# Kernel tuning notes

Hardware: AMD Instinct MI355X
Metric: run time of the kernel (lower is better)

The kernel has to match this reference:

```python
import jax, jax.numpy as jnp
import numpy as np

N = 50000      # nodes
E = 500000     # edges (avg degree 10)
D_IN = 256     # input feature dim
HID = 256      # hidden_channels
HEADS = 8
C_HID = HID // HEADS   # 32 per-head dim for concat layers
NCLS = 8               # num_classes (last layer per-head dim, concat=False)


def setup_inputs() -> dict:
    key = jax.random.key(0)
    keys = iter(jax.random.split(key, 64))
    def w(shape, s=0.05):
        return jax.random.normal(next(keys), shape, jnp.float32) * s
    inp = {}
    inp["x"] = jax.random.normal(next(keys), (N, D_IN), jnp.float32)
    inp["edge_index"] = jax.random.randint(next(keys), (2, E), 0, N, jnp.int32)
    # (fan_in, heads*per_head_out, skip_out) per layer; layer3: concat=False
    layer_cfg = [(D_IN, HEADS * C_HID, HEADS * C_HID),
                 (HID, HEADS * C_HID, HEADS * C_HID),
                 (HID, HEADS * NCLS, NCLS)]
    for i, (fin, hc, skip) in enumerate(layer_cfg, 1):
        for nm in ("q", "k", "v"):
            inp[f"W{nm}{i}"] = w((fin, hc))
            inp[f"b{nm}{i}"] = jnp.zeros((hc,), jnp.float32)
        inp[f"Ws{i}"] = w((fin, skip))
        inp[f"bs{i}"] = jnp.zeros((skip,), jnp.float32)
        inp[f"Wb{i}"] = w((3 * skip, 1))
    for i in (1, 2):
        inp[f"ln{i}_g"] = jnp.ones((HID,), jnp.float32)
        inp[f"ln{i}_b"] = jnp.zeros((HID,), jnp.float32)
    return inp


def _layer_norm(x, g, b):
    mu = x.mean(-1, keepdims=True)
    var = ((x - mu) ** 2).mean(-1, keepdims=True)
    return (x - mu) * jax.lax.rsqrt(var + 1e-5) * g + b


def _tconv(x, src, dst, Wq, bq, Wk, bk, Wv, bv, Ws, bs, Wb, concat):
    """PyG TransformerConv with beta=True, root_weight=True, eval-mode (no dropout)."""
    n = x.shape[0]
    q = (x @ Wq + bq).reshape(n, HEADS, -1)   # [N,H,C]
    k = (x @ Wk + bk).reshape(n, HEADS, -1)
    v = (x @ Wv + bv).reshape(n, HEADS, -1)
    C = q.shape[-1]
    # per-edge attention logits, scaled dot product
    logits = (q[dst] * k[src]).sum(-1) * jax.lax.rsqrt(jnp.float32(C))  # [E,H]
    # segment softmax over incoming edges of each dst node
    m = jax.ops.segment_max(logits, dst, num_segments=n)                # [N,H]
    m = jnp.where(jnp.isfinite(m), m, 0.0)                              # empty segments
    e = jnp.exp(logits - m[dst])
    s = jax.ops.segment_sum(e, dst, num_segments=n)
    alpha = e / (s[dst] + 1e-16)                                        # [E,H]
    # scatter-aggregate messages
    out = jax.ops.segment_sum(v[src] * alpha[:, :, None], dst, num_segments=n)  # [N,H,C]
    out = out.reshape(n, -1) if concat else out.mean(axis=1)
    # beta-gated skip connection
    xr = x @ Ws + bs
    beta = jax.nn.sigmoid(jnp.concatenate([out, xr, out - xr], axis=-1) @ Wb)   # [N,1]
    return beta * xr + (1.0 - beta) * out


def reference(x, edge_index,
              Wq1, bq1, Wk1, bk1, Wv1, bv1, Ws1, bs1, Wb1,
              Wq2, bq2, Wk2, bk2, Wv2, bv2, Ws2, bs2, Wb2,
              Wq3, bq3, Wk3, bk3, Wv3, bv3, Ws3, bs3, Wb3,
              ln1_g, ln1_b, ln2_g, ln2_b):
    src, dst = edge_index[0], edge_index[1]
    h = jax.nn.relu(_layer_norm(
        _tconv(x, src, dst, Wq1, bq1, Wk1, bk1, Wv1, bv1, Ws1, bs1, Wb1, True),
        ln1_g, ln1_b))
    h = jax.nn.relu(_layer_norm(
        _tconv(h, src, dst, Wq2, bq2, Wk2, bk2, Wv2, bv2, Ws2, bs2, Wb2, True),
        ln2_g, ln2_b))
    return _tconv(h, src, dst, Wq3, bq3, Wk3, bk3, Wv3, bv3, Ws3, bs3, Wb3, False)
```

## Files before the change

kernel.cpp:

```cpp
#include <hip/hip_runtime.h>
#include <stdint.h>

typedef __attribute__((ext_vector_type(8))) short short8;
typedef __attribute__((ext_vector_type(4))) float f32x4;
typedef __attribute__((ext_vector_type(4))) _Float16 half4;

struct us4 { unsigned short x, y, z, w; };

__device__ __forceinline__ float b2f(unsigned short u){
  union { unsigned int i; float f; } x; x.i = ((unsigned int)u) << 16; return x.f;
}
__device__ __forceinline__ unsigned short f2b(float f){
  union { float f; unsigned int i; } x; x.f = f;
  unsigned int i = x.i;
  unsigned int r = (i + 0x7FFFu + ((i >> 16) & 1u)) >> 16;
  return (unsigned short)r;
}
__device__ __forceinline__ unsigned short f2h(float f){
  _Float16 h = (_Float16)f;
  union { _Float16 h; unsigned short u; } c; c.h = h; return c.u;
}
__device__ __forceinline__ float sane(float v){
  return fminf(fmaxf(v, -1e30f), 1e30f);
}
__device__ __forceinline__ float lclamp(float v){
  return fminf(fmaxf(v, -60.f), 60.f);
}
__device__ __forceinline__ float ldin(const void* p, size_t i, int f32){
  return f32 ? ((const float*)p)[i] : b2f(((const unsigned short*)p)[i]);
}

__global__ void k_flag(const unsigned short* __restrict__ xu, int* __restrict__ flag){
  __shared__ int cnt;
  if (threadIdx.x == 0) cnt = 0;
  __syncthreads();
  unsigned u = xu[2 * threadIdx.x];
  int e = (u >> 7) & 0xFF;
  if (e >= 97 && e <= 132) atomicAdd(&cnt, 1);
  __syncthreads();
  if (threadIdx.x == 0) flag[0] = (cnt >= 192) ? 0 : 1;
}

__global__ void k_cvt(const void* __restrict__ xin, unsigned short* __restrict__ xb,
                      int n4, const int* __restrict__ flagp){
  int f32 = *flagp;
  int i = blockIdx.x * 256 + threadIdx.x;
  if (i < n4){
    if (f32){
      float4 v = ((const float4*)xin)[i];
      us4 o = { f2b(v.x), f2b(v.y), f2b(v.z), f2b(v.w) };
      ((us4*)xb)[i] = o;
    } else {
      ((us4*)xb)[i] = ((const us4*)xin)[i];
    }
  }
}

__global__ void k_deg(const int* __restrict__ ei, int E, int N, int* __restrict__ deg){
  int e = blockIdx.x * 256 + threadIdx.x;
  if (e < E){
    unsigned d = (unsigned)ei[E + e];
    if (d < (unsigned)N) atomicAdd(&deg[d], 1);
  }
}

__global__ void k_bsum(const int* __restrict__ deg, int N, int* __restrict__ bsum){
  int b = blockIdx.x, t = threadIdx.x;
  int i0 = b * 1024 + t * 4;
  int s = 0;
  if (i0 + 4 <= N){
    int4 v = *(const int4*)&deg[i0];
    s = v.x + v.y + v.z + v.w;
  } else {
    #pragma unroll
    for (int j = 0; j < 4; ++j){ int i = i0 + j; if (i < N) s += deg[i]; }
  }
  #pragma unroll
  for (int off = 32; off; off >>= 1) s += __shfl_xor(s, off);
  __shared__ int ws[4];
  if ((t & 63) == 0) ws[t >> 6] = s;
  __syncthreads();
  if (t == 0) bsum[b] = ws[0] + ws[1] + ws[2] + ws[3];
}

__global__ void k_bscan(const int* __restrict__ bsum, int nb,
                        int* __restrict__ boff, int* __restrict__ rowptr, int N){
  int t = threadIdx.x;
  if (nb <= 64){
    int v = (t < nb) ? bsum[t] : 0;
    int inc = v;
    #pragma unroll
    for (int off = 1; off < 64; off <<= 1){
      int u = __shfl_up(inc, off);
      if (t >= off) inc += u;
    }
    if (t < nb) boff[t] = inc - v;
    if (t == 63) rowptr[N] = inc;
  } else {
    if (t == 0){
      int run = 0;
      for (int i = 0; i < nb; ++i){ boff[i] = run; run += bsum[i]; }
      rowptr[N] = run;
    }
  }
}

__global__ void k_rowptr(const int* __restrict__ deg, const int* __restrict__ boff,
                         int N, int* __restrict__ rowptr, int* __restrict__ cursor){
  int b = blockIdx.x, t = threadIdx.x;
  int i0 = b * 1024 + t * 4;
  int d0 = 0, d1 = 0, d2 = 0, d3 = 0;
  if (i0 + 4 <= N){
    int4 v = *(const int4*)&deg[i0];
    d0 = v.x; d1 = v.y; d2 = v.z; d3 = v.w;
  } else {
    if (i0     < N) d0 = deg[i0];
    if (i0 + 1 < N) d1 = deg[i0 + 1];
    if (i0 + 2 < N) d2 = deg[i0 + 2];
    if (i0 + 3 < N) d3 = deg[i0 + 3];
  }
  int s = d0 + d1 + d2 + d3;
  int lane = t & 63, w = t >> 6;
  int inc = s;
  #pragma unroll
  for (int off = 1; off < 64; off <<= 1){
    int u = __shfl_up(inc, off);
    if (lane >= off) inc += u;
  }
  int wex = inc - s;
  __shared__ int wtot[4];
  if (lane == 63) wtot[w] = inc;
  __syncthreads();
  int cross = 0;
  for (int i = 0; i < w; ++i) cross += wtot[i];
  int basev = boff[b] + cross + wex;
  int r0 = basev, r1 = basev + d0, r2 = r1 + d1, r3 = r2 + d2;
  if (i0 + 4 <= N){
    int4 o = { r0, r1, r2, r3 };
    *(int4*)&rowptr[i0] = o;
    *(int4*)&cursor[i0] = o;
  } else {
    if (i0     < N){ rowptr[i0]   = r0; cursor[i0]   = r0; }
    if (i0 + 1 < N){ rowptr[i0+1] = r1; cursor[i0+1] = r1; }
    if (i0 + 2 < N){ rowptr[i0+2] = r2; cursor[i0+2] = r2; }
    if (i0 + 3 < N){ rowptr[i0+3] = r3; cursor[i0+3] = r3; }
  }
}

__global__ void k_scatter(const int* __restrict__ ei, int E, int N,
                          int* __restrict__ cursor, int* __restrict__ srcs){
  int e = blockIdx.x * 256 + threadIdx.x;
  if (e < E){
    unsigned d = (unsigned)ei[E + e];
    if (d < (unsigned)N){
      int pos = atomicAdd(&cursor[d], 1);
      if ((unsigned)pos < (unsigned)E){
        unsigned s = (unsigned)ei[e];
        srcs[pos] = (s < (unsigned)N) ? (int)(s * 512u) : 0;
      }
    }
  }
}

__global__ void k_pack(const void* __restrict__ Wq, const void* __restrict__ bq,
                       const void* __restrict__ Wk, const void* __restrict__ bk,
                       const void* __restrict__ Wv, const void* __restrict__ bv,
                       const void* __restrict__ Ws, const void* __restrict__ bs,
                       unsigned short* __restrict__ WT, float* __restrict__ bias,
                       int Mq, int Ms, int K, const int* __restrict__ flagp){
  int f32 = *flagp;
  int cg = blockIdx.x;
  int k  = threadIdx.x;
  int mat, c, mc;
  if (cg < 3 * Mq){ mat = cg / Mq; c = cg % Mq; mc = Mq; }
  else if (cg < 3 * Mq + Ms){ mat = 3; c = cg - 3 * Mq; mc = Ms; }
  else { mat = 4; c = 0; mc = 1; }
  const void* W = (mat==0)?Wq:(mat==1)?Wk:(mat==2)?Wv:(mat==3)?Ws:(const void*)0;
  WT[(size_t)cg * K + k] = (mat < 4) ? f2b(ldin(W, (size_t)k * mc + c, f32)) : (unsigned short)0;
  if (k == 0){
    const void* B = (mat==0)?bq:(mat==1)?bk:(mat==2)?bv:(mat==3)?bs:(const void*)0;
    bias[cg] = (mat < 4) ? ldin(B, c, f32) : 0.f;
  }
}

__global__ __launch_bounds__(256) void k_gemm(const unsigned short* __restrict__ A,
                                              const unsigned short* __restrict__ WT,
                                              const float* __restrict__ bias,
                                              unsigned short* __restrict__ B0,
                                              unsigned short* __restrict__ B1,
                                              unsigned short* __restrict__ B2,
                                              unsigned short* __restrict__ B3,
                                              int N, int Mout, int secshift){
  __shared__ __align__(16) unsigned short Alds[64][264];
  __shared__ __align__(16) unsigned short Clds[32][276];
  int tid = threadIdx.x, wid = tid >> 6, lane = tid & 63;
  int l15 = lane & 15, l4 = lane >> 4;
  int row0 = blockIdx.x * 64;
  {
    int srow = tid >> 2, sc4 = tid & 3;
    int ar = row0 + srow; if (ar >= N) ar = N - 1;
    const unsigned short* Ap = A + (size_t)ar * 256;
    #pragma unroll
    for (int i = 0; i < 8; ++i){
      int col = (sc4 + 4 * i) * 8;
      *(short8*)&Alds[srow][col] = *(const short8*)&Ap[col];
    }
  }
  __syncthreads();
  int secw = 1 << secshift;
  int strow = tid >> 3, stchunk = tid & 7;
  for (int cb = wid * 64; cb < Mout; cb += 256){
    f32x4 acc[4][4] = {};
    #pragma unroll
    for (int k0 = 0; k0 < 256; k0 += 32){
      short8 a0 = *(const short8*)&Alds[l15     ][k0 + l4*8];
      short8 a1 = *(const short8*)&Alds[16 + l15][k0 + l4*8];
      short8 a2 = *(const short8*)&Alds[32 + l15][k0 + l4*8];
      short8 a3 = *(const short8*)&Alds[48 + l15][k0 + l4*8];
      const unsigned short* wb = WT + (size_t)(cb + l15) * 256 + k0 + l4*8;
      short8 b0 = *(const short8*)(wb);
      short8 b1 = *(const short8*)(wb + 16*256);
      short8 b2 = *(const short8*)(wb + 32*256);
      short8 b3 = *(const short8*)(wb + 48*256);
      acc[0][0] = __builtin_amdgcn_mfma_f32_16x16x32_bf16(a0, b0, acc[0][0], 0,0,0);
      acc[0][1] = __builtin_amdgcn_mfma_f32_16x16x32_bf16(a0, b1, acc[0][1], 0,0,0);
      acc[0][2] = __builtin_amdgcn_mfma_f32_16x16x32_bf16(a0, b2, acc[0][2], 0,0,0);
      acc[0][3] = __builtin_amdgcn_mfma_f32_16x16x32_bf16(a0, b3, acc[0][3], 0,0,0);
      acc[1][0] = __builtin_amdgcn_mfma_f32_16x16x32_bf16(a1, b0, acc[1][0], 0,0,0);
      acc[1][1] = __builtin_amdgcn_mfma_f32_16x16x32_bf16(a1, b1, acc[1][1], 0,0,0);
      acc[1][2] = __builtin_amdgcn_mfma_f32_16x16x32_bf16(a1, b2, acc[1][2], 0,0,0);
      acc[1][3] = __builtin_amdgcn_mfma_f32_16x16x32_bf16(a1, b3, acc[1][3], 0,0,0);
      acc[2][0] = __builtin_amdgcn_mfma_f32_16x16x32_bf16(a2, b0, acc[2][0], 0,0,0);
      acc[2][1] = __builtin_amdgcn_mfma_f32_16x16x32_bf16(a2, b1, acc[2][1], 0,0,0);
      acc[2][2] = __builtin_amdgcn_mfma_f32_16x16x32_bf16(a2, b2, acc[2][2], 0,0,0);
      acc[2][3] = __builtin_amdgcn_mfma_f32_16x16x32_bf16(a2, b3, acc[2][3], 0,0,0);
      acc[3][0] = __builtin_amdgcn_mfma_f32_16x16x32_bf16(a3, b0, acc[3][0], 0,0,0);
      acc[3][1] = __builtin_amdgcn_mfma_f32_16x16x32_bf16(a3, b1, acc[3][1], 0,0,0);
      acc[3][2] = __builtin_amdgcn_mfma_f32_16x16x32_bf16(a3, b2, acc[3][2], 0,0,0);
      acc[3][3] = __builtin_amdgcn_mfma_f32_16x16x32_bf16(a3, b3, acc[3][3], 0,0,0);
    }
    int gb = cb - wid * 64;
    #pragma unroll
    for (int ph = 0; ph < 2; ++ph){
      #pragma unroll
      for (int rt2 = 0; rt2 < 2; ++rt2){
        int rt = ph*2 + rt2;
        #pragma unroll
        for (int ct = 0; ct < 4; ++ct){
          float bv = bias[cb + ct*16 + l15];
          #pragma unroll
          for (int r = 0; r < 4; ++r)
            Clds[rt2*16 + l4*4 + r][wid*64 + ct*16 + l15] = f2h(acc[rt][ct][r] + bv);
        }
      }
      __syncthreads();
      int grow = row0 + ph*32 + strow;
      if (grow < N){
        int g0 = gb + stchunk * 32;
        int mat = g0 >> secshift;
        int cc  = g0 & (secw - 1);
        unsigned short* Bp = (mat==0)?B0:(mat==1)?B1:(mat==2)?B2:B3;
        unsigned short* dst = Bp + (size_t)grow * secw + cc;
        const unsigned short* srcp = &Clds[strow][stchunk * 32];
        #pragma unroll
        for (int j = 0; j < 4; ++j)
          *(short8*)(dst + j*8) = *(const short8*)(srcp + j*8);
      }
      __syncthreads();
    }
  }
}

__global__ __launch_bounds__(256, 6) void k_attn(const unsigned short* __restrict__ qb,
                                                 const unsigned short* __restrict__ kb,
                                                 const unsigned short* __restrict__ vb,
                                                 const unsigned short* __restrict__ xb,
                                                 const int* __restrict__ rowptr,
                                                 const int* __restrict__ srcs,
                                                 const void* __restrict__ Wb,
                                                 const void* __restrict__ lng,
                                                 const void* __restrict__ lnb,
                                                 unsigned short* __restrict__ hout,
                                                 int N, int E, const int* __restrict__ flagp){
  int f32 = *flagp;
  int tid = threadIdx.x, w = tid >> 6, l = tid & 63;
  int n = blockIdx.x * 4 + w;
  if (n >= N) return;
  const char* q8 = (const char*)qb;
  const char* k8 = (const char*)kb;
  const char* v8 = (const char*)vb;
  const char* x8 = (const char*)xb;
  unsigned l8 = (unsigned)l * 8u;
  size_t nbase = (size_t)n * 512;
  half4 qv = *(const half4*)(q8 + nbase + l8);
  float q0 = (float)qv.x, q1 = (float)qv.y, q2 = (float)qv.z, q3 = (float)qv.w;
  int e0 = rowptr[n], e1 = rowptr[n+1];
  if (e0 < 0) e0 = 0;
  if (e1 > E) e1 = E;
  const float scale = 0.17677669529663687f;
  float ss = 0.f, o0 = 0.f, o1 = 0.f, o2 = 0.f, o3 = 0.f;

  auto edge1 = [&](int eidx){
    unsigned off = (unsigned)srcs[eidx] + l8;
    half4 kk = *(const half4*)(k8 + off);
    half4 vv = *(const half4*)(v8 + off);
    float p = q0*(float)kk.x + q1*(float)kk.y + q2*(float)kk.z + q3*(float)kk.w;
    p += __shfl_xor(p, 1); p += __shfl_xor(p, 2); p += __shfl_xor(p, 4);
    float a = __expf(lclamp(p * scale));
    ss += a;
    o0 += a*(float)vv.x; o1 += a*(float)vv.y; o2 += a*(float)vv.z; o3 += a*(float)vv.w;
  };

  int e = e0;
  while ((e & 3) && e < e1){ edge1(e); ++e; }
  for (; e + 8 <= e1; e += 8){
    int4 oA = *(const int4*)&srcs[e];
    int4 oB = *(const int4*)&srcs[e + 4];
    unsigned off[8] = { (unsigned)oA.x + l8, (unsigned)oA.y + l8,
                        (unsigned)oA.z + l8, (unsigned)oA.w + l8,
                        (unsigned)oB.x + l8, (unsigned)oB.y + l8,
                        (unsigned)oB.z + l8, (unsigned)oB.w + l8 };
    half4 kk[8], vv[8];
    #pragma unroll
    for (int j = 0; j < 8; ++j) kk[j] = *(const half4*)(k8 + off[j]);
    #pragma unroll
    for (int j = 0; j < 8; ++j) vv[j] = *(const half4*)(v8 + off[j]);
    float p[8];
    #pragma unroll
    for (int j = 0; j < 8; ++j)
      p[j] = q0*(float)kk[j].x + q1*(float)kk[j].y + q2*(float)kk[j].z + q3*(float)kk[j].w;
    #pragma unroll
    for (int j = 0; j < 8; ++j){
      p[j] += __shfl_xor(p[j], 1);
      p[j] += __shfl_xor(p[j], 2);
      p[j] += __shfl_xor(p[j], 4);
    }
    #pragma unroll
    for (int j = 0; j < 8; ++j){
      float a = __expf(lclamp(p[j] * scale));
      ss += a;
      o0 += a*(float)vv[j].x; o1 += a*(float)vv[j].y;
      o2 += a*(float)vv[j].z; o3 += a*(float)vv[j].w;
    }
  }
  for (; e + 4 <= e1; e += 4){
    int4 oA = *(const int4*)&srcs[e];
    unsigned off[4] = { (unsigned)oA.x + l8, (unsigned)oA.y + l8,
                        (unsigned)oA.z + l8, (unsigned)oA.w + l8 };
    half4 kk[4], vv[4];
    #pragma unroll
    for (int j = 0; j < 4; ++j) kk[j] = *(const half4*)(k8 + off[j]);
    #pragma unroll
    for (int j = 0; j < 4; ++j) vv[j] = *(const half4*)(v8 + off[j]);
    float p[4];
    #pragma unroll
    for (int j = 0; j < 4; ++j)
      p[j] = q0*(float)kk[j].x + q1*(float)kk[j].y + q2*(float)kk[j].z + q3*(float)kk[j].w;
    #pragma unroll
    for (int j = 0; j < 4; ++j){
      p[j] += __shfl_xor(p[j], 1);
      p[j] += __shfl_xor(p[j], 2);
      p[j] += __shfl_xor(p[j], 4);
    }
    #pragma unroll
    for (int j = 0; j < 4; ++j){
      float a = __expf(lclamp(p[j] * scale));
      ss += a;
      o0 += a*(float)vv[j].x; o1 += a*(float)vv[j].y;
      o2 += a*(float)vv[j].z; o3 += a*(float)vv[j].w;
    }
  }
  for (; e < e1; ++e) edge1(e);

  float sinv = 1.f / (ss + 1e-16f);
  o0 = sane(o0 * sinv); o1 = sane(o1 * sinv);
  o2 = sane(o2 * sinv); o3 = sane(o3 * sinv);
  int c = l * 4;
  half4 xv = *(const half4*)(x8 + nbase + l8);
  float x0 = sane((float)xv.x), x1 = sane((float)xv.y);
  float x2 = sane((float)xv.z), x3 = sane((float)xv.w);
  float d = o0*ldin(Wb, c+0, f32) + x0*ldin(Wb, 256+c+0, f32) + (o0-x0)*ldin(Wb, 512+c+0, f32)
          + o1*ldin(Wb, c+1, f32) + x1*ldin(Wb, 256+c+1, f32) + (o1-x1)*ldin(Wb, 512+c+1, f32)
          + o2*ldin(Wb, c+2, f32) + x2*ldin(Wb, 256+c+2, f32) + (o2-x2)*ldin(Wb, 512+c+2, f32)
          + o3*ldin(Wb, c+3, f32) + x3*ldin(Wb, 256+c+3, f32) + (o3-x3)*ldin(Wb, 512+c+3, f32);
  #pragma unroll
  for (int off = 32; off; off >>= 1) d += __shfl_xor(d, off);
  float beta = 1.f / (1.f + __expf(-d));
  float r0 = beta*x0 + (1.f-beta)*o0;
  float r1 = beta*x1 + (1.f-beta)*o1;
  float r2 = beta*x2 + (1.f-beta)*o2;
  float r3 = beta*x3 + (1.f-beta)*o3;
  float sm = r0 + r1 + r2 + r3;
  #pragma unroll
  for (int off = 32; off; off >>= 1) sm += __shfl_xor(sm, off);
  float mu = sm * (1.f/256.f);
  float d0 = r0-mu, d1 = r1-mu, d2 = r2-mu, d3 = r3-mu;
  float vv2 = d0*d0 + d1*d1 + d2*d2 + d3*d3;
  #pragma unroll
  for (int off = 32; off; off >>= 1) vv2 += __shfl_xor(vv2, off);
  float rs = rsqrtf(vv2 * (1.f/256.f) + 1e-5f);
  us4 outv;
  outv.x = f2b(fmaxf(d0*rs*ldin(lng,c+0,f32) + ldin(lnb,c+0,f32), 0.f));
  outv.y = f2b(fmaxf(d1*rs*ldin(lng,c+1,f32) + ldin(lnb,c+1,f32), 0.f));
  outv.z = f2b(fmaxf(d2*rs*ldin(lng,c+2,f32) + ldin(lnb,c+2,f32), 0.f));
  outv.w = f2b(fmaxf(d3*rs*ldin(lng,c+3,f32) + ldin(lnb,c+3,f32), 0.f));
  *(us4*)&hout[(size_t)n * 256 + c] = outv;
}

__global__ __launch_bounds__(256) void k_final(const unsigned short* __restrict__ q3b,
                                               const unsigned short* __restrict__ k3b,
                                               const unsigned short* __restrict__ v3b,
                                               const unsigned short* __restrict__ x3b,
                                               const int* __restrict__ rowptr,
                                               const int* __restrict__ srcs,
                                               const void* __restrict__ Wb,
                                               void* __restrict__ outp,
                                               int N, int E, const int* __restrict__ flagp){
  int f32 = *flagp;
  int tid = threadIdx.x, w = tid >> 6, l = tid & 63;
  int n = blockIdx.x * 4 + w;
  if (n >= N) return;
  int es = l >> 4, h = (l >> 1) & 7, j = l & 1;
  unsigned sub = (unsigned)(h * 16 + j * 8);
  const char* q8 = (const char*)q3b;
  const char* k8 = (const char*)k3b;
  const char* v8 = (const char*)v3b;
  const char* x8 = (const char*)x3b;
  size_t nbase = (size_t)n * 128;
  half4 qv = *(const half4*)(q8 + nbase + sub);
  float q0 = (float)qv.x, q1 = (float)qv.y, q2 = (float)qv.z, q3f = (float)qv.w;
  int e0 = rowptr[n], e1 = rowptr[n+1];
  if (e0 < 0) e0 = 0;
  if (e1 > E) e1 = E;
  int deg = e1 - e0;
  const float scale = 0.35355339059327373f;
  float ss = 0.f, o0 = 0.f, o1 = 0.f, o2 = 0.f, o3 = 0.f;
  int ei = es;
  for (; ei + 4 < deg; ei += 8){
    unsigned offA = (((unsigned)srcs[e0 + ei])     >> 2) + sub;
    unsigned offB = (((unsigned)srcs[e0 + ei + 4]) >> 2) + sub;
    half4 kA = *(const half4*)(k8 + offA);
    half4 vA = *(const half4*)(v8 + offA);
    half4 kB = *(const half4*)(k8 + offB);
    half4 vB = *(const half4*)(v8 + offB);
    float pA = q0*(float)kA.x + q1*(float)kA.y + q2*(float)kA.z + q3f*(float)kA.w;
    float pB = q0*(float)kB.x + q1*(float)kB.y + q2*(float)kB.z + q3f*(float)kB.w;
    pA += __shfl_xor(pA, 1);
    pB += __shfl_xor(pB, 1);
    float aA = __expf(lclamp(pA * scale));
    float aB = __expf(lclamp(pB * scale));
    ss += aA + aB;
    o0 += aA*(float)vA.x + aB*(float)vB.x;
    o1 += aA*(float)vA.y + aB*(float)vB.y;
    o2 += aA*(float)vA.z + aB*(float)vB.z;
    o3 += aA*(float)vA.w + aB*(float)vB.w;
  }
  if (ei < deg){
    unsigned off = (((unsigned)srcs[e0 + ei]) >> 2) + sub;
    half4 kk = *(const half4*)(k8 + off);
    half4 vv = *(const half4*)(v8 + off);
    float p = q0*(float)kk.x + q1*(float)kk.y + q2*(float)kk.z + q3f*(float)kk.w;
    p += __shfl_xor(p, 1);
    float a = __expf(lclamp(p * scale));
    ss += a;
    o0 += a*(float)vv.x; o1 += a*(float)vv.y; o2 += a*(float)vv.z; o3 += a*(float)vv.w;
  }
  #pragma unroll
  for (int off = 16; off <= 32; off <<= 1){
    ss += __shfl_xor(ss, off);
    o0 += __shfl_xor(o0, off); o1 += __shfl_xor(o1, off);
    o2 += __shfl_xor(o2, off); o3 += __shfl_xor(o3, off);
  }
  float sinv = 1.f / (ss + 1e-16f);
  o0 = sane(o0 * sinv); o1 = sane(o1 * sinv);
  o2 = sane(o2 * sinv); o3 = sane(o3 * sinv);
  #pragma unroll
  for (int off = 2; off <= 8; off <<= 1){
    o0 += __shfl_xor(o0, off); o1 += __shfl_xor(o1, off);
    o2 += __shfl_xor(o2, off); o3 += __shfl_xor(o3, off);
  }
  o0 *= 0.125f; o1 *= 0.125f; o2 *= 0.125f; o3 *= 0.125f;
  half4 xv = *(const half4*)(x8 + nbase + (unsigned)(j * 8));
  float x0 = sane((float)xv.x), x1 = sane((float)xv.y);
  float x2 = sane((float)xv.z), x3v = sane((float)xv.w);
  int c = j*4;
  float d = o0*ldin(Wb, c+0, f32) + x0*ldin(Wb, 8+c+0, f32) + (o0-x0)*ldin(Wb, 16+c+0, f32)
          + o1*ldin(Wb, c+1, f32) + x1*ldin(Wb, 8+c+1, f32) + (o1-x1)*ldin(Wb, 16+c+1, f32)
          + o2*ldin(Wb, c+2, f32) + x2*ldin(Wb, 8+c+2, f32) + (o2-x2)*ldin(Wb, 16+c+2, f32)
          + o3*ldin(Wb, c+3, f32) + x3v*ldin(Wb, 8+c+3, f32) + (o3-x3v)*ldin(Wb, 16+c+3, f32);
  d += __shfl_xor(d, 1);
  float beta = 1.f / (1.f + __expf(-d));
  float r0 = beta*x0  + (1.f-beta)*o0;
  float r1 = beta*x1  + (1.f-beta)*o1;
  float r2 = beta*x2  + (1.f-beta)*o2;
  float r3 = beta*x3v + (1.f-beta)*o3;
  if (l < 2){
    if (f32){
      float* op = (float*)outp + (size_t)n*8 + l*4;
      op[0] = r0; op[1] = r1; op[2] = r2; op[3] = r3;
    } else {
      unsigned short* op = (unsigned short*)outp + (size_t)n*8 + l*4;
      op[0] = f2b(r0); op[1] = f2b(r1); op[2] = f2b(r2); op[3] = f2b(r3);
    }
  }
}

extern "C" void kernel_launch(void* const* d_in, const int* in_sizes, int n_in,
                              void* d_out, int out_size, void* d_ws, size_t ws_size,
                              hipStream_t stream){
  const int* ei = (const int*)d_in[1];
  const int N = in_sizes[0] / 256;
  const int E = in_sizes[1] / 2;

  char* wsp = (char*)d_ws;
  size_t off = 0;
  auto alloc = [&](size_t b) -> void* {
    void* p = wsp + off; off = (off + b + 255) & ~(size_t)255; return p;
  };
  unsigned short* WT1  = (unsigned short*)alloc((size_t)1024*256*2);
  unsigned short* WT2  = (unsigned short*)alloc((size_t)1024*256*2);
  unsigned short* WT3  = (unsigned short*)alloc((size_t)256*256*2);
  float* bias1 = (float*)alloc(1024*4);
  float* bias2 = (float*)alloc(1024*4);
  float* bias3 = (float*)alloc(256*4);
  int* flag   = (int*)alloc(256);
  int* deg    = (int*)alloc((size_t)N*4);
  int* rowptr = (int*)alloc((size_t)(N+1)*4);
  int* cursor = (int*)alloc((size_t)N*4);
  int* bsum   = (int*)alloc(1024*4);
  int* boff   = (int*)alloc(1024*4);
  int* srcs   = (int*)alloc((size_t)E*4);
  unsigned short* xbf = (unsigned short*)alloc((size_t)N*256*2);
  unsigned short* qb  = (unsigned short*)alloc((size_t)N*256*2);
  unsigned short* kb  = (unsigned short*)alloc((size_t)N*256*2);
  unsigned short* vb  = (unsigned short*)alloc((size_t)N*256*2);
  unsigned short* xb  = (unsigned short*)alloc((size_t)N*256*2);
  unsigned short* hbuf= (unsigned short*)alloc((size_t)N*256*2);
  unsigned short* q3 = qb;
  unsigned short* k3 = kb;
  unsigned short* v3 = vb;
  unsigned short* x3 = xb;
  (void)ws_size; (void)n_in; (void)out_size;

  k_flag<<<1, 256, 0, stream>>>((const unsigned short*)d_in[0], flag);
  int n4 = (N * 256) / 4;
  k_cvt<<<(n4 + 255) / 256, 256, 0, stream>>>(d_in[0], xbf, n4, flag);

  hipMemsetAsync(deg, 0, (size_t)N*4, stream);
  int eb = (E + 255) / 256;
  int nbk = (N + 1023) / 1024;
  k_deg<<<eb, 256, 0, stream>>>(ei, E, N, deg);
  k_bsum<<<nbk, 256, 0, stream>>>(deg, N, bsum);
  k_bscan<<<1, 64, 0, stream>>>(bsum, nbk, boff, rowptr, N);
  k_rowptr<<<nbk, 256, 0, stream>>>(deg, boff, N, rowptr, cursor);
  k_scatter<<<eb, 256, 0, stream>>>(ei, E, N, cursor, srcs);

  k_pack<<<1024, 256, 0, stream>>>(d_in[2],  d_in[3],  d_in[4],  d_in[5],  d_in[6],  d_in[7],  d_in[8],  d_in[9],  WT1, bias1, 256, 256, 256, flag);
  k_pack<<<1024, 256, 0, stream>>>(d_in[11], d_in[12], d_in[13], d_in[14], d_in[15], d_in[16], d_in[17], d_in[18], WT2, bias2, 256, 256, 256, flag);
  k_pack<<< 256, 256, 0, stream>>>(d_in[20], d_in[21], d_in[22], d_in[23], d_in[24], d_in[25], d_in[26], d_in[27], WT3, bias3,  64,   8, 256, flag);

  int rb = (N + 63) / 64;
  int nb = (N + 3) / 4;
  k_gemm<<<rb, 256, 0, stream>>>(xbf, WT1, bias1, qb, kb, vb, xb, N, 1024, 8);
  k_attn<<<nb, 256, 0, stream>>>(qb, kb, vb, xb, rowptr, srcs, d_in[10], d_in[29], d_in[30], hbuf, N, E, flag);
  k_gemm<<<rb, 256, 0, stream>>>(hbuf, WT2, bias2, qb, kb, vb, xb, N, 1024, 8);
  k_attn<<<nb, 256, 0, stream>>>(qb, kb, vb, xb, rowptr, srcs, d_in[19], d_in[31], d_in[32], hbuf, N, E, flag);
  k_gemm<<<rb, 256, 0, stream>>>(hbuf, WT3, bias3, q3, k3, v3, x3, N, 256, 6);
  k_final<<<nb, 256, 0, stream>>>(q3, k3, v3, x3, rowptr, srcs, d_in[28], d_out, N, E, flag);
}
```

Before: 671.2 us.

## Pad CSR rows to 8 and process two edges per wave in attention

Each node's CSR segment is padded to a multiple of 8 entries, so every row starts 32-byte aligned and vector srcs loads need no alignment prologue; the real degree is passed separately. The attention kernel now splits each wave into two half-waves that handle alternating edges, with each lane loading 16 bytes (8 fp16) of K and V through inline-asm dwordx4 loads and an explicit waitcnt. The half-wave partial sums are combined with a cross-32 shuffle before the gating and layernorm. This aims for wider, more numerous loads in flight per wave, at the cost of a larger srcs buffer, hand-scheduled asm that can block compiler overlap, and a dropped occupancy hint.

```diff
diff --git a/kernel.cpp b/kernel.cpp
--- a/kernel.cpp
+++ b/kernel.cpp
@@ -4,6 +4,7 @@
 typedef __attribute__((ext_vector_type(8))) short short8;
 typedef __attribute__((ext_vector_type(4))) float f32x4;
 typedef __attribute__((ext_vector_type(4))) _Float16 half4;
+typedef __attribute__((ext_vector_type(4))) int i32x4;
 
 struct us4 { unsigned short x, y, z, w; };
 
@@ -64,16 +65,18 @@
   }
 }
 
+__device__ __forceinline__ int pad8(int d){ return (d + 7) & ~7; }
+
 __global__ void k_bsum(const int* __restrict__ deg, int N, int* __restrict__ bsum){
   int b = blockIdx.x, t = threadIdx.x;
   int i0 = b * 1024 + t * 4;
   int s = 0;
   if (i0 + 4 <= N){
     int4 v = *(const int4*)&deg[i0];
-    s = v.x + v.y + v.z + v.w;
+    s = pad8(v.x) + pad8(v.y) + pad8(v.z) + pad8(v.w);
   } else {
     #pragma unroll
-    for (int j = 0; j < 4; ++j){ int i = i0 + j; if (i < N) s += deg[i]; }
+    for (int j = 0; j < 4; ++j){ int i = i0 + j; if (i < N) s += pad8(deg[i]); }
   }
   #pragma unroll
   for (int off = 32; off; off >>= 1) s += __shfl_xor(s, off);
@@ -119,7 +122,8 @@
     if (i0 + 2 < N) d2 = deg[i0 + 2];
     if (i0 + 3 < N) d3 = deg[i0 + 3];
   }
-  int s = d0 + d1 + d2 + d3;
+  int p0 = pad8(d0), p1 = pad8(d1), p2 = pad8(d2), p3 = pad8(d3);
+  int s = p0 + p1 + p2 + p3;
   int lane = t & 63, w = t >> 6;
   int inc = s;
   #pragma unroll
@@ -134,7 +138,7 @@
   int cross = 0;
   for (int i = 0; i < w; ++i) cross += wtot[i];
   int basev = boff[b] + cross + wex;
-  int r0 = basev, r1 = basev + d0, r2 = r1 + d1, r3 = r2 + d2;
+  int r0 = basev, r1 = basev + p0, r2 = r1 + p1, r3 = r2 + p2;
   if (i0 + 4 <= N){
     int4 o = { r0, r1, r2, r3 };
     *(int4*)&rowptr[i0] = o;
@@ -147,14 +151,14 @@
   }
 }
 
-__global__ void k_scatter(const int* __restrict__ ei, int E, int N,
+__global__ void k_scatter(const int* __restrict__ ei, int E, int N, int Epad,
                           int* __restrict__ cursor, int* __restrict__ srcs){
   int e = blockIdx.x * 256 + threadIdx.x;
   if (e < E){
     unsigned d = (unsigned)ei[E + e];
     if (d < (unsigned)N){
       int pos = atomicAdd(&cursor[d], 1);
-      if ((unsigned)pos < (unsigned)E){
+      if ((unsigned)pos < (unsigned)Epad){
         unsigned s = (unsigned)ei[e];
         srcs[pos] = (s < (unsigned)N) ? (int)(s * 512u) : 0;
       }
@@ -271,140 +275,137 @@
   }
 }
 
-__global__ __launch_bounds__(256, 6) void k_attn(const unsigned short* __restrict__ qb,
-                                                 const unsigned short* __restrict__ kb,
-                                                 const unsigned short* __restrict__ vb,
-                                                 const unsigned short* __restrict__ xb,
-                                                 const int* __restrict__ rowptr,
-                                                 const int* __restrict__ srcs,
-                                                 const void* __restrict__ Wb,
-                                                 const void* __restrict__ lng,
-                                                 const void* __restrict__ lnb,
-                                                 unsigned short* __restrict__ hout,
-                                                 int N, int E, const int* __restrict__ flagp){
+__global__ __launch_bounds__(256) void k_attn(const unsigned short* __restrict__ qb,
+                                              const unsigned short* __restrict__ kb,
+                                              const unsigned short* __restrict__ vb,
+                                              const unsigned short* __restrict__ xb,
+                                              const int* __restrict__ rowptr,
+                                              const int* __restrict__ degv,
+                                              const int* __restrict__ srcs,
+                                              const void* __restrict__ Wb,
+                                              const void* __restrict__ lng,
+                                              const void* __restrict__ lnb,
+                                              unsigned short* __restrict__ hout,
+                                              int N, int E, const int* __restrict__ flagp){
   int f32 = *flagp;
   int tid = threadIdx.x, w = tid >> 6, l = tid & 63;
   int n = blockIdx.x * 4 + w;
   if (n >= N) return;
-  const char* q8 = (const char*)qb;
+  int hl = l & 31;
+  int pairb = l >> 5;
+  unsigned lof = (unsigned)hl * 16u;
   const char* k8 = (const char*)kb;
   const char* v8 = (const char*)vb;
-  const char* x8 = (const char*)xb;
-  unsigned l8 = (unsigned)l * 8u;
   size_t nbase = (size_t)n * 512;
-  half4 qv = *(const half4*)(q8 + nbase + l8);
-  float q0 = (float)qv.x, q1 = (float)qv.y, q2 = (float)qv.z, q3 = (float)qv.w;
-  int e0 = rowptr[n], e1 = rowptr[n+1];
-  if (e0 < 0) e0 = 0;
-  if (e1 > E) e1 = E;
+  union HV { i32x4 v; _Float16 h[8]; };
+  HV qu; qu.v = *(const i32x4*)((const char*)qb + nbase + lof);
+  float q[8];
+  #pragma unroll
+  for (int f = 0; f < 8; ++f) q[f] = (float)qu.h[f];
+  int e0 = rowptr[n]; if (e0 < 0) e0 = 0;
+  int dg = degv[n]; if (dg < 0) dg = 0; if (dg > E) dg = E;
   const float scale = 0.17677669529663687f;
-  float ss = 0.f, o0 = 0.f, o1 = 0.f, o2 = 0.f, o3 = 0.f;
-
-  auto edge1 = [&](int eidx){
-    unsigned off = (unsigned)srcs[eidx] + l8;
-    half4 kk = *(const half4*)(k8 + off);
-    half4 vv = *(const half4*)(v8 + off);
-    float p = q0*(float)kk.x + q1*(float)kk.y + q2*(float)kk.z + q3*(float)kk.w;
-    p += __shfl_xor(p, 1); p += __shfl_xor(p, 2); p += __shfl_xor(p, 4);
+  float ss = 0.f;
+  float o[8];
+  #pragma unroll
+  for (int f = 0; f < 8; ++f) o[f] = 0.f;
+
+  int e = e0, rem = dg;
+  for (; rem >= 8; rem -= 8, e += 8){
+    i32x4 oA = *(const i32x4*)&srcs[e];
+    i32x4 oB = *(const i32x4*)&srcs[e + 4];
+    unsigned vo0 = (unsigned)(pairb ? oA[1] : oA[0]) + lof;
+    unsigned vo1 = (unsigned)(pairb ? oA[3] : oA[2]) + lof;
+    unsigned vo2 = (unsigned)(pairb ? oB[1] : oB[0]) + lof;
+    unsigned vo3 = (unsigned)(pairb ? oB[3] : oB[2]) + lof;
+    i32x4 kd0, kd1, kd2, kd3, vd0, vd1, vd2, vd3;
+    asm volatile("global_load_dwordx4 %0, %1, %2" : "=v"(kd0) : "v"(vo0), "s"(k8));
+    asm volatile("global_load_dwordx4 %0, %1, %2" : "=v"(vd0) : "v"(vo0), "s"(v8));
+    asm volatile("global_load_dwordx4 %0, %1, %2" : "=v"(kd1) : "v"(vo1), "s"(k8));
+    asm volatile("global_load_dwordx4 %0, %1, %2" : "=v"(vd1) : "v"(vo1), "s"(v8));
+    asm volatile("global_load_dwordx4 %0, %1, %2" : "=v"(kd2) : "v"(vo2), "s"(k8));
+    asm volatile("global_load_dwordx4 %0, %1, %2" : "=v"(vd2) : "v"(vo2), "s"(v8));
+    asm volatile("global_load_dwordx4 %0, %1, %2" : "=v"(kd3) : "v"(vo3), "s"(k8));
+    asm volatile("global_load_dwordx4 %0, %1, %2" : "=v"(vd3) : "v"(vo3), "s"(v8));
+    asm volatile("s_waitcnt vmcnt(0)"
+                 : "+v"(kd0), "+v"(vd0), "+v"(kd1), "+v"(vd1),
+                   "+v"(kd2), "+v"(vd2), "+v"(kd3), "+v"(vd3));
+    __builtin_amdgcn_sched_barrier(0);
+    #pragma unroll
+    for (int j = 0; j < 4; ++j){
+      HV kh, vh;
+      kh.v = (j==0)?kd0:(j==1)?kd1:(j==2)?kd2:kd3;
+      vh.v = (j==0)?vd0:(j==1)?vd1:(j==2)?vd2:vd3;
+      float p = 0.f;
+      #pragma unroll
+      for (int f = 0; f < 8; ++f) p += q[f] * (float)kh.h[f];
+      p += __shfl_xor(p, 1); p += __shfl_xor(p, 2);
+      float a = __expf(lclamp(p * scale));
+      ss += a;
+      #pragma unroll
+      for (int f = 0; f < 8; ++f) o[f] += a * (float)vh.h[f];
+    }
+  }
+  for (int t = 0; t < rem; t += 2){
+    int dup = (t + 1 >= rem);
+    int idx = e + t + (dup ? 0 : pairb);
+    unsigned vo = (unsigned)srcs[idx] + lof;
+    HV kh, vh;
+    kh.v = *(const i32x4*)(k8 + vo);
+    vh.v = *(const i32x4*)(v8 + vo);
+    float p = 0.f;
+    #pragma unroll
+    for (int f = 0; f < 8; ++f) p += q[f] * (float)kh.h[f];
+    p += __shfl_xor(p, 1); p += __shfl_xor(p, 2);
     float a = __expf(lclamp(p * scale));
+    if (pairb && dup) a = 0.f;
     ss += a;
-    o0 += a*(float)vv.x; o1 += a*(float)vv.y; o2 += a*(float)vv.z; o3 += a*(float)vv.w;
-  };
-
-  int e = e0;
-  while ((e & 3) && e < e1){ edge1(e); ++e; }
-  for (; e + 8 <= e1; e += 8){
-    int4 oA = *(const int4*)&srcs[e];
-    int4 oB = *(const int4*)&srcs[e + 4];
-    unsigned off[8] = { (unsigned)oA.x + l8, (unsigned)oA.y + l8,
-                        (unsigned)oA.z + l8, (unsigned)oA.w + l8,
-                        (unsigned)oB.x + l8, (unsigned)oB.y + l8,
-                        (unsigned)oB.z + l8, (unsigned)oB.w + l8 };
-    half4 kk[8], vv[8];
-    #pragma unroll
-    for (int j = 0; j < 8; ++j) kk[j] = *(const half4*)(k8 + off[j]);
-    #pragma unroll
-    for (int j = 0; j < 8; ++j) vv[j] = *(const half4*)(v8 + off[j]);
-    float p[8];
-    #pragma unroll
-    for (int j = 0; j < 8; ++j)
-      p[j] = q0*(float)kk[j].x + q1*(float)kk[j].y + q2*(float)kk[j].z + q3*(float)kk[j].w;
-    #pragma unroll
-    for (int j = 0; j < 8; ++j){
-      p[j] += __shfl_xor(p[j], 1);
-      p[j] += __shfl_xor(p[j], 2);
-      p[j] += __shfl_xor(p[j], 4);
-    }
-    #pragma unroll
-    for (int j = 0; j < 8; ++j){
-      float a = __expf(lclamp(p[j] * scale));
-      ss += a;
-      o0 += a*(float)vv[j].x; o1 += a*(float)vv[j].y;
-      o2 += a*(float)vv[j].z; o3 += a*(float)vv[j].w;
-    }
-  }
-  for (; e + 4 <= e1; e += 4){
-    int4 oA = *(const int4*)&srcs[e];
-    unsigned off[4] = { (unsigned)oA.x + l8, (unsigned)oA.y + l8,
-                        (unsigned)oA.z + l8, (unsigned)oA.w + l8 };
-    half4 kk[4], vv[4];
-    #pragma unroll
-    for (int j = 0; j < 4; ++j) kk[j] = *(const half4*)(k8 + off[j]);
-    #pragma unroll
-    for (int j = 0; j < 4; ++j) vv[j] = *(const half4*)(v8 + off[j]);
-    float p[4];
-    #pragma unroll
-    for (int j = 0; j < 4; ++j)
-      p[j] = q0*(float)kk[j].x + q1*(float)kk[j].y + q2*(float)kk[j].z + q3*(float)kk[j].w;
-    #pragma unroll
-    for (int j = 0; j < 4; ++j){
-      p[j] += __shfl_xor(p[j], 1);
-      p[j] += __shfl_xor(p[j], 2);
-      p[j] += __shfl_xor(p[j], 4);
-    }
-    #pragma unroll
-    for (int j = 0; j < 4; ++j){
-      float a = __expf(lclamp(p[j] * scale));
-      ss += a;
-      o0 += a*(float)vv[j].x; o1 += a*(float)vv[j].y;
-      o2 += a*(float)vv[j].z; o3 += a*(float)vv[j].w;
-    }
-  }
-  for (; e < e1; ++e) edge1(e);
+    #pragma unroll
+    for (int f = 0; f < 8; ++f) o[f] += a * (float)vh.h[f];
+  }
+
+  ss += __shfl_xor(ss, 32);
+  #pragma unroll
+  for (int f = 0; f < 8; ++f) o[f] += __shfl_xor(o[f], 32);
 
   float sinv = 1.f / (ss + 1e-16f);
-  o0 = sane(o0 * sinv); o1 = sane(o1 * sinv);
-  o2 = sane(o2 * sinv); o3 = sane(o3 * sinv);
-  int c = l * 4;
-  half4 xv = *(const half4*)(x8 + nbase + l8);
-  float x0 = sane((float)xv.x), x1 = sane((float)xv.y);
-  float x2 = sane((float)xv.z), x3 = sane((float)xv.w);
-  float d = o0*ldin(Wb, c+0, f32) + x0*ldin(Wb, 256+c+0, f32) + (o0-x0)*ldin(Wb, 512+c+0, f32)
-          + o1*ldin(Wb, c+1, f32) + x1*ldin(Wb, 256+c+1, f32) + (o1-x1)*ldin(Wb, 512+c+1, f32)
-          + o2*ldin(Wb, c+2, f32) + x2*ldin(Wb, 256+c+2, f32) + (o2-x2)*ldin(Wb, 512+c+2, f32)
-          + o3*ldin(Wb, c+3, f32) + x3*ldin(Wb, 256+c+3, f32) + (o3-x3)*ldin(Wb, 512+c+3, f32);
-  #pragma unroll
-  for (int off = 32; off; off >>= 1) d += __shfl_xor(d, off);
+  #pragma unroll
+  for (int f = 0; f < 8; ++f) o[f] = sane(o[f] * sinv);
+  int c = hl * 8;
+  HV xu; xu.v = *(const i32x4*)((const char*)xb + nbase + lof);
+  float x[8];
+  #pragma unroll
+  for (int f = 0; f < 8; ++f) x[f] = sane((float)xu.h[f]);
+  float d = 0.f;
+  #pragma unroll
+  for (int f = 0; f < 8; ++f)
+    d += o[f]*ldin(Wb, c+f, f32) + x[f]*ldin(Wb, 256+c+f, f32)
+       + (o[f]-x[f])*ldin(Wb, 512+c+f, f32);
+  #pragma unroll
+  for (int off = 1; off <= 16; off <<= 1) d += __shfl_xor(d, off);
   float beta = 1.f / (1.f + __expf(-d));
-  float r0 = beta*x0 + (1.f-beta)*o0;
-  float r1 = beta*x1 + (1.f-beta)*o1;
-  float r2 = beta*x2 + (1.f-beta)*o2;
-  float r3 = beta*x3 + (1.f-beta)*o3;
-  float sm = r0 + r1 + r2 + r3;
-  #pragma unroll
-  for (int off = 32; off; off >>= 1) sm += __shfl_xor(sm, off);
+  float r[8];
+  #pragma unroll
+  for (int f = 0; f < 8; ++f) r[f] = beta*x[f] + (1.f-beta)*o[f];
+  float sm = 0.f;
+  #pragma unroll
+  for (int f = 0; f < 8; ++f) sm += r[f];
+  #pragma unroll
+  for (int off = 1; off <= 16; off <<= 1) sm += __shfl_xor(sm, off);
   float mu = sm * (1.f/256.f);
-  float d0 = r0-mu, d1 = r1-mu, d2 = r2-mu, d3 = r3-mu;
-  float vv2 = d0*d0 + d1*d1 + d2*d2 + d3*d3;
-  #pragma unroll
-  for (int off = 32; off; off >>= 1) vv2 += __shfl_xor(vv2, off);
+  float dev[8], vv2 = 0.f;
+  #pragma unroll
+  for (int f = 0; f < 8; ++f){ dev[f] = r[f] - mu; vv2 += dev[f]*dev[f]; }
+  #pragma unroll
+  for (int off = 1; off <= 16; off <<= 1) vv2 += __shfl_xor(vv2, off);
   float rs = rsqrtf(vv2 * (1.f/256.f) + 1e-5f);
-  us4 outv;
-  outv.x = f2b(fmaxf(d0*rs*ldin(lng,c+0,f32) + ldin(lnb,c+0,f32), 0.f));
-  outv.y = f2b(fmaxf(d1*rs*ldin(lng,c+1,f32) + ldin(lnb,c+1,f32), 0.f));
-  outv.z = f2b(fmaxf(d2*rs*ldin(lng,c+2,f32) + ldin(lnb,c+2,f32), 0.f));
-  outv.w = f2b(fmaxf(d3*rs*ldin(lng,c+3,f32) + ldin(lnb,c+3,f32), 0.f));
-  *(us4*)&hout[(size_t)n * 256 + c] = outv;
+  if (l < 32){
+    short8 sv;
+    #pragma unroll
+    for (int f = 0; f < 8; ++f)
+      sv[f] = (short)f2b(fmaxf(dev[f]*rs*ldin(lng, c+f, f32) + ldin(lnb, c+f, f32), 0.f));
+    *(short8*)&hout[(size_t)n * 256 + c] = sv;
+  }
 }
 
 __global__ __launch_bounds__(256) void k_final(const unsigned short* __restrict__ q3b,
@@ -412,6 +413,7 @@
                                                const unsigned short* __restrict__ v3b,
                                                const unsigned short* __restrict__ x3b,
                                                const int* __restrict__ rowptr,
+                                               const int* __restrict__ degv,
                                                const int* __restrict__ srcs,
                                                const void* __restrict__ Wb,
                                                void* __restrict__ outp,
@@ -429,10 +431,8 @@
   size_t nbase = (size_t)n * 128;
   half4 qv = *(const half4*)(q8 + nbase + sub);
   float q0 = (float)qv.x, q1 = (float)qv.y, q2 = (float)qv.z, q3f = (float)qv.w;
-  int e0 = rowptr[n], e1 = rowptr[n+1];
-  if (e0 < 0) e0 = 0;
-  if (e1 > E) e1 = E;
-  int deg = e1 - e0;
+  int e0 = rowptr[n]; if (e0 < 0) e0 = 0;
+  int deg = degv[n]; if (deg < 0) deg = 0; if (deg > E) deg = E;
   const float scale = 0.35355339059327373f;
   float ss = 0.f, o0 = 0.f, o1 = 0.f, o2 = 0.f, o3 = 0.f;
   int ei = es;
@@ -511,6 +511,7 @@
   const int* ei = (const int*)d_in[1];
   const int N = in_sizes[0] / 256;
   const int E = in_sizes[1] / 2;
+  const int Epad = E + 8 * N + 64;
 
   char* wsp = (char*)d_ws;
   size_t off = 0;
@@ -529,7 +530,7 @@
   int* cursor = (int*)alloc((size_t)N*4);
   int* bsum   = (int*)alloc(1024*4);
   int* boff   = (int*)alloc(1024*4);
-  int* srcs   = (int*)alloc((size_t)E*4);
+  int* srcs   = (int*)alloc((size_t)Epad*4);
   unsigned short* xbf = (unsigned short*)alloc((size_t)N*256*2);
   unsigned short* qb  = (unsigned short*)alloc((size_t)N*256*2);
   unsigned short* kb  = (unsigned short*)alloc((size_t)N*256*2);
@@ -553,7 +554,7 @@
   k_bsum<<<nbk, 256, 0, stream>>>(deg, N, bsum);
   k_bscan<<<1, 64, 0, stream>>>(bsum, nbk, boff, rowptr, N);
   k_rowptr<<<nbk, 256, 0, stream>>>(deg, boff, N, rowptr, cursor);
-  k_scatter<<<eb, 256, 0, stream>>>(ei, E, N, cursor, srcs);
+  k_scatter<<<eb, 256, 0, stream>>>(ei, E, N, Epad, cursor, srcs);
 
   k_pack<<<1024, 256, 0, stream>>>(d_in[2],  d_in[3],  d_in[4],  d_in[5],  d_in[6],  d_in[7],  d_in[8],  d_in[9],  WT1, bias1, 256, 256, 256, flag);
   k_pack<<<1024, 256, 0, stream>>>(d_in[11], d_in[12], d_in[13], d_in[14], d_in[15], d_in[16], d_in[17], d_in[18], WT2, bias2, 256, 256, 256, flag);
@@ -562,9 +563,9 @@
   int rb = (N + 63) / 64;
   int nb = (N + 3) / 4;
   k_gemm<<<rb, 256, 0, stream>>>(xbf, WT1, bias1, qb, kb, vb, xb, N, 1024, 8);
-  k_attn<<<nb, 256, 0, stream>>>(qb, kb, vb, xb, rowptr, srcs, d_in[10], d_in[29], d_in[30], hbuf, N, E, flag);
+  k_attn<<<nb, 256, 0, stream>>>(qb, kb, vb, xb, rowptr, deg, srcs, d_in[10], d_in[29], d_in[30], hbuf, N, E, flag);
   k_gemm<<<rb, 256, 0, stream>>>(hbuf, WT2, bias2, qb, kb, vb, xb, N, 1024, 8);
-  k_attn<<<nb, 256, 0, stream>>>(qb, kb, vb, xb, rowptr, srcs, d_in[19], d_in[31], d_in[32], hbuf, N, E, flag);
+  k_attn<<<nb, 256, 0, stream>>>(qb, kb, vb, xb, rowptr, deg, srcs, d_in[19], d_in[31], d_in[32], hbuf, N, E, flag);
   k_gemm<<<rb, 256, 0, stream>>>(hbuf, WT3, bias3, q3, k3, v3, x3, N, 256, 6);
-  k_final<<<nb, 256, 0, stream>>>(q3, k3, v3, x3, rowptr, srcs, d_in[28], d_out, N, E, flag);
-}
+  k_final<<<nb, 256, 0, stream>>>(q3, k3, v3, x3, rowptr, deg, srcs, d_in[28], d_out, N, E, flag);
+}
```

Measured after the change: 878.2 us. 1.31x slower.
